# Kernel tuning notes

Measured on AMD Instinct MI355X. Metric: run time of the kernel, lower is better.

The kernel has to match this reference:

```python
import jax, jax.numpy as jnp
import numpy as np

B, H, W, S, C = 16, 128, 128, 4, 64
SC = S * C
SK_ITERS, SK_EPS = 20, 1e-6


def setup_inputs() -> dict:
    key = jax.random.key(0)
    ks = jax.random.split(key, 12)
    x = jax.random.normal(ks[0], (B, H, W, S, C), dtype=jnp.float32)
    # torch Linear weights are [out, in], kaiming-uniform-ish scale ~ 1/sqrt(in)
    w_pre = jax.random.normal(ks[1], (S, SC), dtype=jnp.float32) / np.sqrt(SC)
    w_post = jax.random.normal(ks[2], (S, SC), dtype=jnp.float32) / np.sqrt(SC)
    w_res = jax.random.normal(ks[3], (S * S, SC), dtype=jnp.float32) / np.sqrt(SC)
    b_pre = jax.random.normal(ks[4], (1, S), dtype=jnp.float32) * 0.01
    b_res = jax.random.normal(ks[5], (S * S,), dtype=jnp.float32) * 0.01
    b_post = jax.random.normal(ks[6], (1, S), dtype=jnp.float32) * 0.01
    alpha_pre = jax.random.normal(ks[7], (1,), dtype=jnp.float32) * 0.01
    alpha_res = jax.random.normal(ks[8], (1,), dtype=jnp.float32) * 0.01
    alpha_post = jax.random.normal(ks[9], (1,), dtype=jnp.float32) * 0.01
    rms_w = jnp.ones((SC,), dtype=jnp.float32)
    # conv kernel HWIO for 3x3 same-padded Conv2d(C, C, bias=False)
    conv_w = jax.random.normal(ks[10], (3, 3, C, C), dtype=jnp.float32) / np.sqrt(9 * C)
    return {"x": x, "w_pre": w_pre, "w_post": w_post, "w_res": w_res,
            "b_pre": b_pre, "b_res": b_res, "b_post": b_post,
            "alpha_pre": alpha_pre, "alpha_res": alpha_res, "alpha_post": alpha_post,
            "rms_w": rms_w, "conv_w": conv_w}


def _sinkhorn(h_tilde):
    # h_tilde: [B,H,W,S,S]; stable softmax-style shift then 20 row/col rescales
    h = h_tilde - h_tilde.max(axis=(-2, -1), keepdims=True)
    h = jnp.exp(h)
    def body(_, h):
        h = h / (h.sum(axis=-2, keepdims=True) + SK_EPS)
        h = h / (h.sum(axis=-1, keepdims=True) + SK_EPS)
        return h
    return jax.lax.fori_loop(0, SK_ITERS, body, h)


def reference(x, w_pre, w_post, w_res, b_pre, b_res, b_post,
              alpha_pre, alpha_res, alpha_post, rms_w, conv_w):
    s = b_pre.shape[-1]
    x_arrow = x.reshape(*x.shape[:-2], -1)           # [B,H,W,S*C]
    eps = jnp.finfo(x.dtype).eps                     # torch RMSNorm default eps
    x_norm = x_arrow * jax.lax.rsqrt(jnp.mean(x_arrow * x_arrow, axis=-1, keepdims=True) + eps)
    x_norm = x_norm * rms_w

    h_tilde_pre = alpha_pre * (x_norm @ w_pre.T) + b_pre          # [B,H,W,S]
    h_tilde_post = alpha_post * (x_norm @ w_post.T) + b_post       # [B,H,W,S]
    h_tilde_res = alpha_res * (x_norm @ w_res.T).reshape(*x.shape[:-2], s, s) \
                  + b_res.reshape(s, s)                            # [B,H,W,S,S]

    h_pre = jax.nn.sigmoid(h_tilde_pre)                            # [B,H,W,S]
    h_res = _sinkhorn(h_tilde_res)                                 # [B,H,W,S,S]
    h_post = 2.0 * jax.nn.sigmoid(h_tilde_post)                    # [B,H,W,S]

    # x_pre = h_pre @ x (pre-mix across streams) -> [B,H,W,C]
    x_pre = jnp.einsum('bhws,bhwsc->bhwc', h_pre, x)
    # layer: Conv2d(C,C,3,padding=1,bias=False), applied in NHWC directly
    layer_out = jax.lax.conv_general_dilated(
        x_pre, conv_w, window_strides=(1, 1), padding='SAME',
        dimension_numbers=('NHWC', 'HWIO', 'NHWC'))                # [B,H,W,C]

    out = jnp.einsum('bhwst,bhwtc->bhwsc', h_res, x) \
          + h_post[..., :, None] * layer_out[..., None, :]         # [B,H,W,S,C]
    return out
```

## Files before the change

### kernel.cpp

```cpp
#include <hip/hip_runtime.h>
#include <cstdint>
#include <cstring>

typedef unsigned int u32;
typedef unsigned short u16;
typedef __attribute__((ext_vector_type(8))) __bf16 bf16x8;
typedef __attribute__((ext_vector_type(4))) float f32x4;

#define DEV static __device__ __forceinline__

DEV float bf2f(u16 v){ u32 u = ((u32)v)<<16; float f; __builtin_memcpy(&f,&u,4); return f; }
DEV u16 f2bf(float f){ u32 u; __builtin_memcpy(&u,&f,4); u32 r = u + 0x7fffu + ((u>>16)&1u); return (u16)(r>>16); }
DEV void unpk(u32 v, float& lo, float& hi){
  u32 a = v<<16; u32 b = v & 0xffff0000u;
  __builtin_memcpy(&lo,&a,4); __builtin_memcpy(&hi,&b,4);
}
DEV u32 pk2(float lo, float hi){ return (u32)f2bf(lo) | (((u32)f2bf(hi))<<16); }
DEV float fsigm(float x){ return __builtin_amdgcn_rcpf(1.f + __expf(-x)); }
DEV f32x4 MFMA16(uint4 a, uint4 b, f32x4 c){
  return __builtin_amdgcn_mfma_f32_16x16x32_bf16(
      __builtin_bit_cast(bf16x8, a), __builtin_bit_cast(bf16x8, b), c, 0, 0, 0);
}

DEV bool detect_bf16(const void* rmsw){ return ((const u16*)rmsw)[0] == 0x3F80u; }

DEV u32 rnd1(u32 f){ return (f + 0x7fffu + ((f>>16)&1u)) >> 16; }
DEV u32 rnd2(u32 lo, u32 hi){ return rnd1(lo) | (rnd1(hi)<<16); }

DEV uint4 load8(const void* p, size_t idx8, bool bf){
  if (bf) return ((const uint4*)p)[idx8];
  const uint4* q = (const uint4*)p;
  uint4 a = q[2*idx8], b = q[2*idx8+1];
  return make_uint4(rnd2(a.x,a.y), rnd2(a.z,a.w), rnd2(b.x,b.y), rnd2(b.z,b.w));
}
DEV void store8(void* p, size_t idx8, bool bf, const float* v){
  if (bf){
    ((uint4*)p)[idx8] = make_uint4(pk2(v[0],v[1]),pk2(v[2],v[3]),pk2(v[4],v[5]),pk2(v[6],v[7]));
  } else {
    float4* q = (float4*)p;
    q[2*idx8]   = make_float4(v[0],v[1],v[2],v[3]);
    q[2*idx8+1] = make_float4(v[4],v[5],v[6],v[7]);
  }
}
DEV float ldsc(const void* p, int i, bool bf){
  return bf ? bf2f(((const u16*)p)[i]) : ((const float*)p)[i];
}

__global__ __launch_bounds__(256) void prepack_kernel(
    const void* __restrict__ wpre, const void* __restrict__ wpost,
    const void* __restrict__ wres, const void* __restrict__ rmsw,
    const void* __restrict__ convw, u16* __restrict__ wsW, u16* __restrict__ wsC)
{
  const bool bf = detect_bf16(rmsw);
  int tid = blockIdx.x*256 + threadIdx.x;
  if (tid < 8192){
    int i = tid & 7, lane = (tid>>3)&63, nt = (tid>>9)&1, kk = tid>>10;
    int j = nt*16 + (lane&15);
    int k = kk*32 + ((lane>>4)<<3) + i;
    float v = 0.f;
    if (j < 4)       v = ldsc(wpre, j*256+k, bf);
    else if (j < 8)  v = ldsc(wpost, (j-4)*256+k, bf);
    else if (j < 24) v = ldsc(wres, (j-8)*256+k, bf);
    v *= ldsc(rmsw, k, bf);
    wsW[tid] = f2bf(v);
  }
  if (tid < 36864){
    int i = tid & 7, lane = (tid>>3)&63, nt = (tid>>9)&3, kk = tid>>11;
    int co = nt*16 + (lane&15);
    int k = kk*32 + ((lane>>4)<<3) + i;
    wsC[tid] = f2bf(ldsc(convw, k*64+co, bf));
  }
}

__global__ __launch_bounds__(256,4) void mHC_fused_kernel(
    const void* __restrict__ x,
    const void* __restrict__ bpre, const void* __restrict__ bres, const void* __restrict__ bpost,
    const void* __restrict__ apre, const void* __restrict__ ares, const void* __restrict__ apost,
    const void* __restrict__ rmsw,
    const u16* __restrict__ wsW, const u16* __restrict__ wsC,
    void* __restrict__ out)
{
  __shared__ __align__(16) u16 s_xpre[10*18*68];
  __shared__ __align__(16) u16 s_h[128*20];
  __shared__ __align__(16) u16 s_hpre[4][64];
  __shared__ __align__(16) u16 s_L[4][16*68];

  const bool bf = detect_bf16(rmsw);
  const int tid = threadIdx.x;
  const int wave = tid>>6, lane = tid&63;
  const int mm = lane&15, q = lane>>4;
  const int blk = blockIdx.x;
  const int bimg = blk>>7, ty = (blk>>3)&15, tx = blk&7;
  const size_t xb8 = (size_t)bimg*16384*32;
  const int gy0 = ty*8-1, gx0 = tx*16-1;

  const float a_pre = ldsc(apre,0,bf), a_res = ldsc(ares,0,bf), a_post = ldsc(apost,0,bf);
  const float al0 = (mm<4)? a_pre : (mm<8)? a_post : a_res;
  const float bi0 = (mm<4)? ldsc(bpre,mm,bf) : (mm<8)? ldsc(bpost,mm-4,bf) : ldsc(bres,mm-8,bf);
  const float al1 = a_res;
  const float bi1 = (mm<8)? ldsc(bres,mm+8,bf) : 0.f;

  const uint4* wWv = reinterpret_cast<const uint4*>(wsW);
  const uint4* wCv = reinterpret_cast<const uint4*>(wsC);

  #pragma unroll
  for (int i=0;i<2;i++){
    const int iy = wave*2 + i;
    const int gy = ty*8 + iy, gx = tx*16 + mm;
    const size_t p8 = xb8 + (size_t)(gy*128 + gx)*32;
    uint4 A[8];
    #pragma unroll
    for (int kk=0;kk<8;kk++) A[kk] = load8(x, p8 + kk*4+q, bf);

    float ssq = 0.f;
    #pragma unroll
    for (int kk=0;kk<8;kk++){
      const u32 vv[4] = {A[kk].x,A[kk].y,A[kk].z,A[kk].w};
      #pragma unroll
      for (int w2=0;w2<4;w2++){ float lo,hi; unpk(vv[w2],lo,hi);
        ssq = __builtin_fmaf(lo,lo,ssq); ssq = __builtin_fmaf(hi,hi,ssq); }
    }
    ssq += __shfl_xor(ssq,16);
    ssq += __shfl_xor(ssq,32);
    const float scale = __builtin_amdgcn_rsqf(ssq*(1.f/256.f) + 1.1920928955078125e-07f);
    float rs[4];
    #pragma unroll
    for (int r=0;r<4;r++) rs[r] = __shfl(scale, q*4+r);

    f32x4 D0 = {0.f,0.f,0.f,0.f}, D1 = {0.f,0.f,0.f,0.f};
    #pragma unroll
    for (int kk=0;kk<8;kk++){
      D0 = MFMA16(A[kk], wWv[(kk*2+0)*64+lane], D0);
      D1 = MFMA16(A[kk], wWv[(kk*2+1)*64+lane], D1);
    }
    #pragma unroll
    for (int r=0;r<4;r++){
      const float ht0 = __builtin_fmaf(al0*rs[r], D0[r], bi0);
      const float ht1 = __builtin_fmaf(al1*rs[r], D1[r], bi1);
      if (mm < 4) s_hpre[wave][(q*4+r)*4+mm] = f2bf(fsigm(ht0));
      const int pid = iy*16 + (q*4+r);
      if (mm < 8) s_h[pid*20 + mm+8] = f2bf(ht1);
      else        s_h[pid*20 + mm-8] = f2bf(ht0);
      if (mm>=4 && mm<8) s_h[pid*20 + 12 + mm] = f2bf(2.f*fsigm(ht0));
    }
    __builtin_amdgcn_wave_barrier();
    {
      float hp[4];
      { const uint2 hv = *reinterpret_cast<const uint2*>(&s_hpre[wave][mm*4]);
        unpk(hv.x, hp[0], hp[1]); unpk(hv.y, hp[2], hp[3]); }
      float xa[8] = {0,0,0,0,0,0,0,0}, xb[8] = {0,0,0,0,0,0,0,0};
      #pragma unroll
      for (int kk=0;kk<8;kk++){
        const float h = hp[kk>>1];
        const u32 vv[4] = {A[kk].x,A[kk].y,A[kk].z,A[kk].w};
        #pragma unroll
        for (int w2=0;w2<4;w2++){
          float lo,hi; unpk(vv[w2],lo,hi);
          if (kk&1){ xb[2*w2]  =__builtin_fmaf(h,lo,xb[2*w2]);  xb[2*w2+1]=__builtin_fmaf(h,hi,xb[2*w2+1]); }
          else     { xa[2*w2]  =__builtin_fmaf(h,lo,xa[2*w2]);  xa[2*w2+1]=__builtin_fmaf(h,hi,xa[2*w2+1]); }
        }
      }
      const int pix = (iy+1)*18 + (mm+1);
      uint2* dA = reinterpret_cast<uint2*>(&s_xpre[pix*68 + 8*q]);
      dA[0] = make_uint2(pk2(xa[0],xa[1]), pk2(xa[2],xa[3]));
      dA[1] = make_uint2(pk2(xa[4],xa[5]), pk2(xa[6],xa[7]));
      uint2* dB = reinterpret_cast<uint2*>(&s_xpre[pix*68 + 32 + 8*q]);
      dB[0] = make_uint2(pk2(xb[0],xb[1]), pk2(xb[2],xb[3]));
      dB[1] = make_uint2(pk2(xb[4],xb[5]), pk2(xb[6],xb[7]));
    }
    __builtin_amdgcn_wave_barrier();
  }

  {
    const int hx = wave*16 + mm;
    const bool pv = hx < 52;
    int ey, ex;
    if (hx < 18)      { ey = 0;       ex = hx;      }
    else if (hx < 36) { ey = 9;       ex = hx-18;   }
    else if (hx < 44) { ey = hx-35;   ex = 0;       }
    else              { ey = hx-43;   ex = 17;      }
    const int gy = gy0+ey, gx = gx0+ex;
    const bool inimg = pv && ((u32)gy < 128u) && ((u32)gx < 128u);
    const size_t p8 = xb8 + (size_t)(u32)(gy*128 + gx)*32;

    uint4 A[8];
    #pragma unroll
    for (int kk=0;kk<8;kk++){
      uint4 v = make_uint4(0u,0u,0u,0u);
      if (inimg) v = load8(x, p8 + kk*4+q, bf);
      A[kk] = v;
    }
    float ssq = 0.f;
    #pragma unroll
    for (int kk=0;kk<8;kk++){
      const u32 vv[4] = {A[kk].x,A[kk].y,A[kk].z,A[kk].w};
      #pragma unroll
      for (int w2=0;w2<4;w2++){ float lo,hi; unpk(vv[w2],lo,hi);
        ssq = __builtin_fmaf(lo,lo,ssq); ssq = __builtin_fmaf(hi,hi,ssq); }
    }
    ssq += __shfl_xor(ssq,16);
    ssq += __shfl_xor(ssq,32);
    const float scale = __builtin_amdgcn_rsqf(ssq*(1.f/256.f) + 1.1920928955078125e-07f);
    float rs[4];
    #pragma unroll
    for (int r=0;r<4;r++) rs[r] = __shfl(scale, q*4+r);

    f32x4 D0 = {0.f,0.f,0.f,0.f};
    #pragma unroll
    for (int kk=0;kk<8;kk++) D0 = MFMA16(A[kk], wWv[(kk*2+0)*64+lane], D0);

    #pragma unroll
    for (int r=0;r<4;r++){
      if (mm < 4){
        const float ht0 = __builtin_fmaf(al0*rs[r], D0[r], bi0);
        s_hpre[wave][(q*4+r)*4+mm] = f2bf(fsigm(ht0));
      }
    }
    __builtin_amdgcn_wave_barrier();
    if (pv){
      float hp[4];
      { const uint2 hv = *reinterpret_cast<const uint2*>(&s_hpre[wave][mm*4]);
        unpk(hv.x, hp[0], hp[1]); unpk(hv.y, hp[2], hp[3]); }
      float xa[8] = {0,0,0,0,0,0,0,0}, xb[8] = {0,0,0,0,0,0,0,0};
      #pragma unroll
      for (int kk=0;kk<8;kk++){
        const float h = hp[kk>>1];
        const u32 vv[4] = {A[kk].x,A[kk].y,A[kk].z,A[kk].w};
        #pragma unroll
        for (int w2=0;w2<4;w2++){
          float lo,hi; unpk(vv[w2],lo,hi);
          if (kk&1){ xb[2*w2]  =__builtin_fmaf(h,lo,xb[2*w2]);  xb[2*w2+1]=__builtin_fmaf(h,hi,xb[2*w2+1]); }
          else     { xa[2*w2]  =__builtin_fmaf(h,lo,xa[2*w2]);  xa[2*w2+1]=__builtin_fmaf(h,hi,xa[2*w2+1]); }
        }
      }
      const int pix = ey*18 + ex;
      uint2* dA = reinterpret_cast<uint2*>(&s_xpre[pix*68 + 8*q]);
      dA[0] = make_uint2(pk2(xa[0],xa[1]), pk2(xa[2],xa[3]));
      dA[1] = make_uint2(pk2(xa[4],xa[5]), pk2(xa[6],xa[7]));
      uint2* dB = reinterpret_cast<uint2*>(&s_xpre[pix*68 + 32 + 8*q]);
      dB[0] = make_uint2(pk2(xb[0],xb[1]), pk2(xb[2],xb[3]));
      dB[1] = make_uint2(pk2(xb[4],xb[5]), pk2(xb[6],xb[7]));
    }
    __builtin_amdgcn_wave_barrier();
  }
  __syncthreads();

  if (tid < 128){
    const int p = tid;
    float h[16];
    const uint2* h2 = reinterpret_cast<const uint2*>(&s_h[p*20]);
    #pragma unroll
    for (int e=0;e<4;e++){ const uint2 v = h2[e];
      unpk(v.x,h[4*e],h[4*e+1]); unpk(v.y,h[4*e+2],h[4*e+3]); }
    float mx = h[0];
    #pragma unroll
    for (int e=1;e<16;e++) mx = fmaxf(mx,h[e]);
    #pragma unroll
    for (int e=0;e<16;e++) h[e] = __expf(h[e]-mx);
    for (int it=0; it<20; ++it){
      #pragma unroll
      for (int t=0;t<4;t++){
        const float rc = __builtin_amdgcn_rcpf((h[t]+h[4+t])+(h[8+t]+h[12+t]) + 1e-6f);
        h[t]*=rc; h[4+t]*=rc; h[8+t]*=rc; h[12+t]*=rc;
      }
      #pragma unroll
      for (int s=0;s<4;s++){
        const float rc = __builtin_amdgcn_rcpf((h[4*s]+h[4*s+1])+(h[4*s+2]+h[4*s+3]) + 1e-6f);
        h[4*s]*=rc; h[4*s+1]*=rc; h[4*s+2]*=rc; h[4*s+3]*=rc;
      }
    }
    uint2* hw = reinterpret_cast<uint2*>(&s_h[p*20]);
    #pragma unroll
    for (int e=0;e<4;e++) hw[e] = make_uint2(pk2(h[4*e],h[4*e+1]), pk2(h[4*e+2],h[4*e+3]));
  }
  __syncthreads();

  #pragma unroll
  for (int i=0;i<2;i++){
    const int py = wave*2+i;
    f32x4 D[4];
    #pragma unroll
    for (int nt=0;nt<4;nt++) D[nt] = (f32x4){0.f,0.f,0.f,0.f};
    #pragma unroll
    for (int kk=0;kk<18;kk++){
      const int tq  = 4*kk+q;
      const int tap = tq>>3;
      const int ci0 = (tq&7)*8;
      const int dy = tap/3, dx = tap-3*dy;
      const int pix = (py+dy)*18 + (mm+dx);
      const uint2* a2 = reinterpret_cast<const uint2*>(&s_xpre[pix*68 + ci0]);
      const uint2 alo = a2[0], ahi = a2[1];
      const uint4 av = make_uint4(alo.x, alo.y, ahi.x, ahi.y);
      #pragma unroll
      for (int nt=0;nt<4;nt++)
        D[nt] = MFMA16(av, wCv[(kk*4+nt)*64+lane], D[nt]);
    }
    const int gy = ty*8+py, gx = tx*16+mm;
    const size_t p8 = xb8 + (size_t)(gy*128+gx)*32;
    uint4 A[8];
    #pragma unroll
    for (int kk=0;kk<8;kk++) A[kk] = load8(x, p8 + kk*4+q, bf);

    __builtin_amdgcn_wave_barrier();
    #pragma unroll
    for (int nt=0;nt<4;nt++)
      #pragma unroll
      for (int r=0;r<4;r++)
        s_L[wave][(q*4+r)*68 + nt*16 + mm] = f2bf(D[nt][r]);
    __builtin_amdgcn_wave_barrier();

    float xa[4][8], xb[4][8];
    #pragma unroll
    for (int t=0;t<4;t++){
      const u32 va[4] = {A[2*t].x,A[2*t].y,A[2*t].z,A[2*t].w};
      const u32 vb[4] = {A[2*t+1].x,A[2*t+1].y,A[2*t+1].z,A[2*t+1].w};
      #pragma unroll
      for (int w2=0;w2<4;w2++){
        unpk(va[w2], xa[t][2*w2], xa[t][2*w2+1]);
        unpk(vb[w2], xb[t][2*w2], xb[t][2*w2+1]);
      }
    }
    const int pid = py*16+mm;
    float hr[16], hpo[4];
    {
      const uint2* h2 = reinterpret_cast<const uint2*>(&s_h[pid*20]);
      #pragma unroll
      for (int e=0;e<4;e++){ const uint2 v = h2[e];
        unpk(v.x,hr[4*e],hr[4*e+1]); unpk(v.y,hr[4*e+2],hr[4*e+3]); }
      const uint2 v4 = h2[4];
      unpk(v4.x,hpo[0],hpo[1]); unpk(v4.y,hpo[2],hpo[3]);
    }
    float LA[8], LB[8];
    {
      const uint2* lA = reinterpret_cast<const uint2*>(&s_L[wave][mm*68 + 8*q]);
      const uint2* lB = reinterpret_cast<const uint2*>(&s_L[wave][mm*68 + 32 + 8*q]);
      const uint2 a0v=lA[0], a1v=lA[1], b0v=lB[0], b1v=lB[1];
      unpk(a0v.x,LA[0],LA[1]); unpk(a0v.y,LA[2],LA[3]);
      unpk(a1v.x,LA[4],LA[5]); unpk(a1v.y,LA[6],LA[7]);
      unpk(b0v.x,LB[0],LB[1]); unpk(b0v.y,LB[2],LB[3]);
      unpk(b1v.x,LB[4],LB[5]); unpk(b1v.y,LB[6],LB[7]);
    }
    const size_t ob8 = ((size_t)bimg*16384 + (size_t)(gy*128+gx))*32;
    #pragma unroll
    for (int s=0;s<4;s++){
      float oA[8], oB[8];
      #pragma unroll
      for (int j2=0;j2<8;j2++){ oA[j2]=hpo[s]*LA[j2]; oB[j2]=hpo[s]*LB[j2]; }
      #pragma unroll
      for (int t=0;t<4;t++){
        const float w0 = hr[4*s+t];
        #pragma unroll
        for (int j2=0;j2<8;j2++){
          oA[j2]=__builtin_fmaf(w0,xa[t][j2],oA[j2]);
          oB[j2]=__builtin_fmaf(w0,xb[t][j2],oB[j2]);
        }
      }
      store8(out, ob8 + s*8 + q,     bf, oA);
      store8(out, ob8 + s*8 + 4 + q, bf, oB);
    }
  }
}

extern "C" void kernel_launch(void* const* d_in, const int* in_sizes, int n_in,
                              void* d_out, int out_size, void* d_ws, size_t ws_size,
                              hipStream_t stream)
{
  const void* x     = d_in[0];
  const void* wpre  = d_in[1];
  const void* wpost = d_in[2];
  const void* wres  = d_in[3];
  const void* bpre  = d_in[4];
  const void* bres  = d_in[5];
  const void* bpost = d_in[6];
  const void* apre  = d_in[7];
  const void* ares  = d_in[8];
  const void* apost = d_in[9];
  const void* rmsw  = d_in[10];
  const void* convw = d_in[11];
  u16* wsW = (u16*)d_ws;
  u16* wsC = wsW + 8192;

  hipLaunchKernelGGL(prepack_kernel, dim3(144), dim3(256), 0, stream,
                     wpre, wpost, wres, rmsw, convw, wsW, wsC);
  hipLaunchKernelGGL(mHC_fused_kernel, dim3(2048), dim3(256), 0, stream,
                     x, bpre, bres, bpost, apre, ares, apost, rmsw, wsW, wsC, d_out);
}
```

Baseline: 662.9 us.

## Split fused kernel into front (norm/projections/sinkhorn) and back (conv/mix) passes

Splits the single fused kernel into two. A front kernel computes RMSNorm, the projections, sigmoid gates, Sinkhorn and x_pre per pixel, then writes x_pre and the mixing weights to a workspace. A back kernel loads halo tiles of x_pre, runs the 3x3 conv with MFMA and does the final residual mix. This likely removes redundant halo recomputation of x_pre and the projections that the fused kernel did, at the cost of an extra round trip of the x_pre and h buffers through global memory and a second launch. The old fused path remains as a fallback when the workspace is too small.

```diff
diff --git a/kernel.cpp b/kernel.cpp
--- a/kernel.cpp
+++ b/kernel.cpp
@@ -69,6 +69,246 @@
     int co = nt*16 + (lane&15);
     int k = kk*32 + ((lane>>4)<<3) + i;
     wsC[tid] = f2bf(ldsc(convw, k*64+co, bf));
+  }
+}
+
+__global__ __launch_bounds__(256,6) void front_kernel(
+    const void* __restrict__ x,
+    const void* __restrict__ bpre, const void* __restrict__ bres, const void* __restrict__ bpost,
+    const void* __restrict__ apre, const void* __restrict__ ares, const void* __restrict__ apost,
+    const void* __restrict__ rmsw,
+    const u16* __restrict__ wsW, u16* __restrict__ xpre_ws, u16* __restrict__ h_ws)
+{
+  __shared__ __align__(16) u16 s_h[4][64*24];
+  __shared__ __align__(16) u16 s_hpre[4][64];
+
+  const bool bf = detect_bf16(rmsw);
+  const int tid = threadIdx.x;
+  const int wave = tid>>6, lane = tid&63;
+  const int mm = lane&15, q = lane>>4;
+  const int pxbase = blockIdx.x*256 + wave*64;
+
+  const float a_pre = ldsc(apre,0,bf), a_res = ldsc(ares,0,bf), a_post = ldsc(apost,0,bf);
+  const float al0 = (mm<4)? a_pre : (mm<8)? a_post : a_res;
+  const float bi0 = (mm<4)? ldsc(bpre,mm,bf) : (mm<8)? ldsc(bpost,mm-4,bf) : ldsc(bres,mm-8,bf);
+  const float al1 = a_res;
+  const float bi1 = (mm<8)? ldsc(bres,mm+8,bf) : 0.f;
+
+  const uint4* wWv = reinterpret_cast<const uint4*>(wsW);
+
+  #pragma unroll
+  for (int i=0;i<4;i++){
+    const int px = pxbase + i*16 + mm;
+    const size_t p8 = (size_t)px*32;
+    uint4 A[8];
+    #pragma unroll
+    for (int kk=0;kk<8;kk++) A[kk] = load8(x, p8 + kk*4+q, bf);
+
+    float ssq = 0.f;
+    #pragma unroll
+    for (int kk=0;kk<8;kk++){
+      const u32 vv[4] = {A[kk].x,A[kk].y,A[kk].z,A[kk].w};
+      #pragma unroll
+      for (int w2=0;w2<4;w2++){ float lo,hi; unpk(vv[w2],lo,hi);
+        ssq = __builtin_fmaf(lo,lo,ssq); ssq = __builtin_fmaf(hi,hi,ssq); }
+    }
+    ssq += __shfl_xor(ssq,16);
+    ssq += __shfl_xor(ssq,32);
+    const float scale = __builtin_amdgcn_rsqf(ssq*(1.f/256.f) + 1.1920928955078125e-07f);
+    float rs[4];
+    #pragma unroll
+    for (int r=0;r<4;r++) rs[r] = __shfl(scale, q*4+r);
+
+    f32x4 D0 = {0.f,0.f,0.f,0.f}, D1 = {0.f,0.f,0.f,0.f};
+    #pragma unroll
+    for (int kk=0;kk<8;kk++){
+      D0 = MFMA16(A[kk], wWv[(kk*2+0)*64+lane], D0);
+      D1 = MFMA16(A[kk], wWv[(kk*2+1)*64+lane], D1);
+    }
+    #pragma unroll
+    for (int r=0;r<4;r++){
+      const float ht0 = __builtin_fmaf(al0*rs[r], D0[r], bi0);
+      const float ht1 = __builtin_fmaf(al1*rs[r], D1[r], bi1);
+      if (mm < 4) s_hpre[wave][(q*4+r)*4+mm] = f2bf(fsigm(ht0));
+      const int pl = i*16 + q*4 + r;
+      if (mm < 8) s_h[wave][pl*24 + mm+8] = f2bf(ht1);
+      else        s_h[wave][pl*24 + mm-8] = f2bf(ht0);
+      if (mm>=4 && mm<8) s_h[wave][pl*24 + 12 + mm] = f2bf(2.f*fsigm(ht0));
+    }
+    __builtin_amdgcn_wave_barrier();
+    {
+      float hp[4];
+      { const uint2 hv = *reinterpret_cast<const uint2*>(&s_hpre[wave][mm*4]);
+        unpk(hv.x, hp[0], hp[1]); unpk(hv.y, hp[2], hp[3]); }
+      float xa[8] = {0,0,0,0,0,0,0,0}, xb[8] = {0,0,0,0,0,0,0,0};
+      #pragma unroll
+      for (int kk=0;kk<8;kk++){
+        const float h = hp[kk>>1];
+        const u32 vv[4] = {A[kk].x,A[kk].y,A[kk].z,A[kk].w};
+        #pragma unroll
+        for (int w2=0;w2<4;w2++){
+          float lo,hi; unpk(vv[w2],lo,hi);
+          if (kk&1){ xb[2*w2]  =__builtin_fmaf(h,lo,xb[2*w2]);  xb[2*w2+1]=__builtin_fmaf(h,hi,xb[2*w2+1]); }
+          else     { xa[2*w2]  =__builtin_fmaf(h,lo,xa[2*w2]);  xa[2*w2+1]=__builtin_fmaf(h,hi,xa[2*w2+1]); }
+        }
+      }
+      uint4* dA = reinterpret_cast<uint4*>(&xpre_ws[(size_t)px*64 + 8*q]);
+      *dA = make_uint4(pk2(xa[0],xa[1]), pk2(xa[2],xa[3]), pk2(xa[4],xa[5]), pk2(xa[6],xa[7]));
+      uint4* dB = reinterpret_cast<uint4*>(&xpre_ws[(size_t)px*64 + 32 + 8*q]);
+      *dB = make_uint4(pk2(xb[0],xb[1]), pk2(xb[2],xb[3]), pk2(xb[4],xb[5]), pk2(xb[6],xb[7]));
+    }
+    __builtin_amdgcn_wave_barrier();
+  }
+
+  {
+    const int pl = lane;
+    const size_t px = (size_t)pxbase + pl;
+    const uint4* h4 = reinterpret_cast<const uint4*>(&s_h[wave][pl*24]);
+    const uint4 ha = h4[0], hb = h4[1];
+    const uint2 hpost = *reinterpret_cast<const uint2*>(&s_h[wave][pl*24+16]);
+    float h[16];
+    unpk(ha.x,h[0],h[1]);  unpk(ha.y,h[2],h[3]);  unpk(ha.z,h[4],h[5]);  unpk(ha.w,h[6],h[7]);
+    unpk(hb.x,h[8],h[9]);  unpk(hb.y,h[10],h[11]); unpk(hb.z,h[12],h[13]); unpk(hb.w,h[14],h[15]);
+    float mx = h[0];
+    #pragma unroll
+    for (int e=1;e<16;e++) mx = fmaxf(mx,h[e]);
+    #pragma unroll
+    for (int e=0;e<16;e++) h[e] = __expf(h[e]-mx);
+    for (int it=0; it<20; ++it){
+      #pragma unroll
+      for (int t=0;t<4;t++){
+        const float rc = __builtin_amdgcn_rcpf((h[t]+h[4+t])+(h[8+t]+h[12+t]) + 1e-6f);
+        h[t]*=rc; h[4+t]*=rc; h[8+t]*=rc; h[12+t]*=rc;
+      }
+      #pragma unroll
+      for (int s=0;s<4;s++){
+        const float rc = __builtin_amdgcn_rcpf((h[4*s]+h[4*s+1])+(h[4*s+2]+h[4*s+3]) + 1e-6f);
+        h[4*s]*=rc; h[4*s+1]*=rc; h[4*s+2]*=rc; h[4*s+3]*=rc;
+      }
+    }
+    uint2* g = reinterpret_cast<uint2*>(&h_ws[px*20]);
+    g[0] = make_uint2(pk2(h[0],h[1]),  pk2(h[2],h[3]));
+    g[1] = make_uint2(pk2(h[4],h[5]),  pk2(h[6],h[7]));
+    g[2] = make_uint2(pk2(h[8],h[9]),  pk2(h[10],h[11]));
+    g[3] = make_uint2(pk2(h[12],h[13]),pk2(h[14],h[15]));
+    g[4] = hpost;
+  }
+}
+
+__global__ __launch_bounds__(256,4) void back_kernel(
+    const void* __restrict__ x, const void* __restrict__ rmsw,
+    const u16* __restrict__ wsC, const u16* __restrict__ xpre_ws,
+    const u16* __restrict__ h_ws, void* __restrict__ out)
+{
+  __shared__ __align__(16) u16 s_xpre[10*18*68];
+  __shared__ __align__(16) u16 s_L[4][16*68];
+
+  const bool bf = detect_bf16(rmsw);
+  const int tid = threadIdx.x;
+  const int wave = tid>>6, lane = tid&63;
+  const int mm = lane&15, q = lane>>4;
+  const int blk = blockIdx.x;
+  const int bimg = blk>>7, ty = (blk>>3)&15, tx = blk&7;
+  const size_t xb8 = (size_t)bimg*16384*32;
+  const int gy0 = ty*8-1, gx0 = tx*16-1;
+
+  const uint4* wCv = reinterpret_cast<const uint4*>(wsC);
+
+  for (int idx = tid; idx < 1440; idx += 256){
+    const int row = idx/144;
+    const int off = idx - row*144;
+    const int pxr = off>>3, sub = off&7;
+    const int gy = gy0+row, gx = gx0+pxr;
+    uint4 v = make_uint4(0u,0u,0u,0u);
+    if ((u32)gy < 128u && (u32)gx < 128u)
+      v = ((const uint4*)xpre_ws)[((size_t)bimg*16384 + (size_t)(gy*128+gx))*8 + sub];
+    *reinterpret_cast<uint4*>(&s_xpre[(row*18+pxr)*68 + sub*8]) = v;
+  }
+  __syncthreads();
+
+  #pragma unroll
+  for (int i=0;i<2;i++){
+    const int py = wave*2+i;
+    f32x4 D[4];
+    #pragma unroll
+    for (int nt=0;nt<4;nt++) D[nt] = (f32x4){0.f,0.f,0.f,0.f};
+    #pragma unroll
+    for (int kk=0;kk<18;kk++){
+      const int tq  = 4*kk+q;
+      const int tap = tq>>3;
+      const int ci0 = (tq&7)*8;
+      const int dy = tap/3, dx = tap-3*dy;
+      const int pix = (py+dy)*18 + (mm+dx);
+      const uint2* a2 = reinterpret_cast<const uint2*>(&s_xpre[pix*68 + ci0]);
+      const uint2 alo = a2[0], ahi = a2[1];
+      const uint4 av = make_uint4(alo.x, alo.y, ahi.x, ahi.y);
+      #pragma unroll
+      for (int nt=0;nt<4;nt++)
+        D[nt] = MFMA16(av, wCv[(kk*4+nt)*64+lane], D[nt]);
+    }
+    const int gy = ty*8+py, gx = tx*16+mm;
+    const size_t p8 = xb8 + (size_t)(gy*128+gx)*32;
+    uint4 A[8];
+    #pragma unroll
+    for (int kk=0;kk<8;kk++) A[kk] = load8(x, p8 + kk*4+q, bf);
+    const size_t pidg = (size_t)bimg*16384 + (size_t)(gy*128+gx);
+    const uint2* hg = reinterpret_cast<const uint2*>(&h_ws[pidg*20]);
+    const uint2 hv0=hg[0], hv1=hg[1], hv2=hg[2], hv3=hg[3], hv4=hg[4];
+
+    __builtin_amdgcn_wave_barrier();
+    #pragma unroll
+    for (int nt=0;nt<4;nt++)
+      #pragma unroll
+      for (int r=0;r<4;r++)
+        s_L[wave][(q*4+r)*68 + nt*16 + mm] = f2bf(D[nt][r]);
+    __builtin_amdgcn_wave_barrier();
+
+    float xa[4][8], xb[4][8];
+    #pragma unroll
+    for (int t=0;t<4;t++){
+      const u32 va[4] = {A[2*t].x,A[2*t].y,A[2*t].z,A[2*t].w};
+      const u32 vb[4] = {A[2*t+1].x,A[2*t+1].y,A[2*t+1].z,A[2*t+1].w};
+      #pragma unroll
+      for (int w2=0;w2<4;w2++){
+        unpk(va[w2], xa[t][2*w2], xa[t][2*w2+1]);
+        unpk(vb[w2], xb[t][2*w2], xb[t][2*w2+1]);
+      }
+    }
+    float hr[16], hpo[4];
+    unpk(hv0.x,hr[0],hr[1]);   unpk(hv0.y,hr[2],hr[3]);
+    unpk(hv1.x,hr[4],hr[5]);   unpk(hv1.y,hr[6],hr[7]);
+    unpk(hv2.x,hr[8],hr[9]);   unpk(hv2.y,hr[10],hr[11]);
+    unpk(hv3.x,hr[12],hr[13]); unpk(hv3.y,hr[14],hr[15]);
+    unpk(hv4.x,hpo[0],hpo[1]); unpk(hv4.y,hpo[2],hpo[3]);
+
+    float LA[8], LB[8];
+    {
+      const uint2* lA = reinterpret_cast<const uint2*>(&s_L[wave][mm*68 + 8*q]);
+      const uint2* lB = reinterpret_cast<const uint2*>(&s_L[wave][mm*68 + 32 + 8*q]);
+      const uint2 a0v=lA[0], a1v=lA[1], b0v=lB[0], b1v=lB[1];
+      unpk(a0v.x,LA[0],LA[1]); unpk(a0v.y,LA[2],LA[3]);
+      unpk(a1v.x,LA[4],LA[5]); unpk(a1v.y,LA[6],LA[7]);
+      unpk(b0v.x,LB[0],LB[1]); unpk(b0v.y,LB[2],LB[3]);
+      unpk(b1v.x,LB[4],LB[5]); unpk(b1v.y,LB[6],LB[7]);
+    }
+    const size_t ob8 = (pidg)*32;
+    #pragma unroll
+    for (int s=0;s<4;s++){
+      float oA[8], oB[8];
+      #pragma unroll
+      for (int j2=0;j2<8;j2++){ oA[j2]=hpo[s]*LA[j2]; oB[j2]=hpo[s]*LB[j2]; }
+      #pragma unroll
+      for (int t=0;t<4;t++){
+        const float w0 = hr[4*s+t];
+        #pragma unroll
+        for (int j2=0;j2<8;j2++){
+          oA[j2]=__builtin_fmaf(w0,xa[t][j2],oA[j2]);
+          oB[j2]=__builtin_fmaf(w0,xb[t][j2],oB[j2]);
+        }
+      }
+      store8(out, ob8 + s*8 + q,     bf, oA);
+      store8(out, ob8 + s*8 + 4 + q, bf, oB);
+    }
   }
 }
 
@@ -380,8 +620,24 @@
   u16* wsW = (u16*)d_ws;
   u16* wsC = wsW + 8192;
 
+  const size_t OFF_XPRE = 131072;
+  const size_t SZ_XPRE  = (size_t)262144*64*2;
+  const size_t OFF_H    = OFF_XPRE + SZ_XPRE;
+  const size_t SZ_H     = (size_t)262144*20*2;
+  const size_t NEED     = OFF_H + SZ_H;
+
   hipLaunchKernelGGL(prepack_kernel, dim3(144), dim3(256), 0, stream,
                      wpre, wpost, wres, rmsw, convw, wsW, wsC);
-  hipLaunchKernelGGL(mHC_fused_kernel, dim3(2048), dim3(256), 0, stream,
-                     x, bpre, bres, bpost, apre, ares, apost, rmsw, wsW, wsC, d_out);
-}
+
+  if (ws_size >= NEED){
+    u16* xpre = (u16*)((char*)d_ws + OFF_XPRE);
+    u16* hws  = (u16*)((char*)d_ws + OFF_H);
+    hipLaunchKernelGGL(front_kernel, dim3(1024), dim3(256), 0, stream,
+                       x, bpre, bres, bpost, apre, ares, apost, rmsw, wsW, xpre, hws);
+    hipLaunchKernelGGL(back_kernel, dim3(2048), dim3(256), 0, stream,
+                       x, rmsw, wsC, xpre, hws, d_out);
+  } else {
+    hipLaunchKernelGGL(mHC_fused_kernel, dim3(2048), dim3(256), 0, stream,
+                       x, bpre, bres, bpost, apre, ares, apost, rmsw, wsW, wsC, d_out);
+  }
+}
```

Measured after the change: 717.9 us. 1.08x slower.
